# Kernel optimization log

Hardware: AMD Instinct MI355X
Metric: run time of the kernel (lower is better)

## Reference

```python
import jax, jax.numpy as jnp
import numpy as np

B, L, S, H, E = 2, 2048, 2048, 16, 64
EPS = 1e-8


def setup_inputs() -> dict:
    key = jax.random.key(0)
    k1, k2, k3, k4, k5 = jax.random.split(key, 5)
    query = jax.random.normal(k1, (B, L, H, E), dtype=jnp.float32)
    key_t = jax.random.normal(k2, (B, S, H, E), dtype=jnp.float32)
    value = jax.random.normal(k3, (B, S, H, E), dtype=jnp.float32)
    mask_miss_k = jax.random.randint(k4, (B, S, 1), 0, 2).astype(bool)
    mask_miss_q = jax.random.randint(k5, (B, L, 1), 0, 2).astype(bool)
    # monotone per-batch positions -> standard causal structure
    pos = jnp.broadcast_to(jnp.arange(L, dtype=jnp.int32)[None, :, None], (B, L, 1))
    return {"query": query, "key": key_t, "value": value,
            "mask_miss_k": mask_miss_k, "mask_miss_q": mask_miss_q,
            "pos": pos, "causal_mask": 1}


def reference(query, key, value, mask_miss_k, mask_miss_q, pos, causal_mask):
    # query: (B,L,H,E); key/value: (B,S,H,E)
    E_ = query.shape[-1]
    scale = 1.0 / np.sqrt(E_)
    scores = jnp.einsum('blhe,bshe->bhls', query, key)  # (B,H,L,S)
    if causal_mask:
        p = pos[..., 0]  # (B,L)
        causal_add = jnp.where(p[:, None, :] > p[:, :, None],
                               -jnp.inf, 0.0).astype(scores.dtype)  # (B,L,S)
        scores = scores + causal_add[:, None, :, :]
    # additive -inf masks for missing keys / queries
    m_k = jnp.where(mask_miss_k[..., 0][:, None, None, :], -jnp.inf, 0.0).astype(scores.dtype)
    m_q = jnp.where(mask_miss_q[..., 0][:, None, :, None], -jnp.inf, 0.0).astype(scores.dtype)
    # NOTE: scale multiplies (scores + M_k) exactly as in the original
    att = jnp.maximum(jax.nn.softmax(scale * (scores + m_k), axis=-1) + m_q, 0.0)
    # entropy of (post-relu, possibly unnormalized) attention weights
    entropy = -jnp.sum(att * jnp.log(jnp.clip(att, EPS, None)), axis=-1)  # (B,H,L)
    entropy = jnp.nan_to_num(entropy, nan=0.0)
    A = jnp.nan_to_num(att)  # dropout p=0 -> identity, then nan_to_num
    V = jnp.einsum('bhls,bshd->blhd', A, value)  # (B,L,H,E)
    return V, A, entropy
```

## Files before the change

### kernel.cpp

```cpp
#include <hip/hip_runtime.h>

#define BB 2
#define LL 2048
#define SS 2048
#define HH 16
#define EE 64
#define HE (HH*EE)
#define BL 128
#define TS 64
#define NT2 32
#define SCALEF 0.125f
#define NEGBIG (-1e30f)

typedef __bf16 bf8 __attribute__((ext_vector_type(8)));
typedef float f4v __attribute__((ext_vector_type(4)));
typedef unsigned int u32;
typedef unsigned short u16;

#define V_ELEMS  ((size_t)BB*LL*HH*EE)
#define A_BASE   (V_ELEMS)
#define ENT_BASE (A_BASE + (size_t)BB*HH*LL*SS)

__device__ __forceinline__ u16 bfb(float f) {
    u32 u = __builtin_bit_cast(u32, f);
    return (u16)((u + 0x7fffu + ((u >> 16) & 1u)) >> 16);
}
__device__ __forceinline__ int swz8(int r) { return (((r) & 7) ^ (((r) >> 3) & 7)) << 4; }

__device__ __forceinline__ f4v mfma16(bf8 a, bf8 b, f4v c) {
    return __builtin_amdgcn_mfma_f32_16x16x32_bf16(a, b, c, 0, 0, 0);
}
__device__ __forceinline__ int maskv(const void* p, int i, int isB) {
    return isB ? (int)((const unsigned char*)p)[i] : ((const int*)p)[i];
}
__device__ __forceinline__ void barrier_lds() {
    asm volatile("s_waitcnt lgkmcnt(0)" ::: "memory");
    __builtin_amdgcn_s_barrier();
    asm volatile("" ::: "memory");
}
__device__ __forceinline__ uint4 pack8(float4 f0, float4 f1) {
    uint4 wv;
    wv.x = bfb(f0.x) | ((u32)bfb(f0.y) << 16);
    wv.y = bfb(f0.z) | ((u32)bfb(f0.w) << 16);
    wv.z = bfb(f1.x) | ((u32)bfb(f1.y) << 16);
    wv.w = bfb(f1.z) | ((u32)bfb(f1.w) << 16);
    return wv;
}
__device__ __forceinline__ void st_out(float v, float* p) { *p = v; }
__device__ __forceinline__ void st_out4(f4v v, float* p) { *(f4v*)(void*)p = v; }

__device__ __forceinline__ void stage128x64(const float* __restrict__ src,
                                            char* lds, int tid) {
    const int r = tid >> 2, seg = tid & 3;
    const float* rp = src + (size_t)r * HE + seg * 16;
    float4 f0 = *(const float4*)(rp + 0);
    float4 f1 = *(const float4*)(rp + 4);
    float4 f2 = *(const float4*)(rp + 8);
    float4 f3 = *(const float4*)(rp + 12);
    const int base = r * 128 + seg * 32;
    *(uint4*)(void*)(lds + ((base +  0) ^ swz8(r))) = pack8(f0, f1);
    *(uint4*)(void*)(lds + ((base + 16) ^ swz8(r))) = pack8(f2, f3);
}

__global__ __launch_bounds__(512) void k_fused(
    const float* __restrict__ Qg, const float* __restrict__ Kg, const float* __restrict__ Vg,
    const void* __restrict__ mk, const void* __restrict__ mq,
    float* __restrict__ outF)
{
    __shared__ __align__(16) char ldsP[16384];
    __shared__ __align__(16) char ldsK[2][8192];
    __shared__ __align__(16) char ldsVT[2][8192];
    __shared__ float ldsKM[SS];
    __shared__ int sFlag;

    const int blk = blockIdx.x;
    const int bh  = (blk & 7) + (((blk >> 3) & 3) << 3);
    const int pair = blk >> 5;
    const int b = bh >> 4, h = bh & 15;
    const int tid = threadIdx.x;
    const int w = tid >> 6, lane = tid & 63, g = lane >> 4, le = lane & 15;

    int isB;
    {
        const unsigned char* c = (const unsigned char*)mk;
        unsigned acc = 0;
        #pragma unroll
        for (int j = 0; j < 8; ++j) {
            const int off = tid + j * 512;
            if (off & 3) acc |= c[off];
        }
        if (tid == 0) sFlag = 0;
        __syncthreads();
        if (acc) atomicOr(&sFlag, 1);
        __syncthreads();
        isB = sFlag;
    }
    for (int i = tid; i < SS; i += 512)
        ldsKM[i] = maskv(mk, b * SS + i, isB) ? NEGBIG : 0.f;

    const float* Qb = Qg + (size_t)b * LL * HE + h * EE;
    const float* Kb = Kg + (size_t)b * SS * HE + h * EE;
    const float* Vb = Vg + (size_t)b * SS * HE + h * EE;

    const int kr = tid >> 3, ksg = tid & 7;
    const float* kbase = Kb + (size_t)kr * HE + ksg * 8;
    const int koff = (kr * 128 + ksg * 16) ^ swz8(kr);
    const int vrp = tid >> 4, vei = tid & 15;
    const float* vbase = Vb + (size_t)(2 * vrp) * HE + vei * 4;

    for (int bi = 0; bi < 2; ++bi) {
        const int band = bi ? (15 - pair) : pair;
        const int l0 = band * BL;
        const int lbase = l0 + w * 16 + g * 4;
        const int whi = l0 + w * 16 + 15;
        const int ntile = 2 * (band + 1);

        stage128x64(Qb + (size_t)l0 * HE, ldsP, tid);
        __syncthreads();
        const int qr = w * 16 + le;
        bf8 qf0 = *(const bf8*)(void*)(ldsP + ((qr * 128 +  0 + g * 16) ^ swz8(qr)));
        bf8 qf1 = *(const bf8*)(void*)(ldsP + ((qr * 128 + 64 + g * 16) ^ swz8(qr)));
        barrier_lds();

        float M[4], D[4], T[4];
        #pragma unroll
        for (int r = 0; r < 4; ++r) { M[r] = NEGBIG; D[r] = 0.f; T[r] = 0.f; }

        float4 ka = *(const float4*)(kbase);
        float4 kb2 = *(const float4*)(kbase + 4);
        *(uint4*)(void*)(&ldsK[0][0] + koff) = pack8(ka, kb2);
        if (ntile > 1) {
            const float* kp = kbase + (size_t)TS * HE;
            ka = *(const float4*)(kp); kb2 = *(const float4*)(kp + 4);
        }
        barrier_lds();
        int cur = 0;

        for (int st = 0; st < ntile; ++st) {
            const int s0 = st * TS;
            if (st + 1 < ntile) {
                *(uint4*)(void*)(&ldsK[cur ^ 1][0] + koff) = pack8(ka, kb2);
                if (st + 2 < ntile) {
                    const float* kp = kbase + (size_t)(st + 2) * TS * HE;
                    ka = *(const float4*)(kp); kb2 = *(const float4*)(kp + 4);
                }
            }
            if (s0 <= whi) {
                f4v acc[4];
                float tm[4] = {NEGBIG, NEGBIG, NEGBIG, NEGBIG};
                #pragma unroll
                for (int cb = 0; cb < 4; ++cb) {
                    const int sr = cb * 16 + le;
                    bf8 k0 = *(const bf8*)(void*)(&ldsK[cur][0] + ((sr * 128 +  0 + g * 16) ^ swz8(sr)));
                    bf8 k1 = *(const bf8*)(void*)(&ldsK[cur][0] + ((sr * 128 + 64 + g * 16) ^ swz8(sr)));
                    f4v a = {0.f, 0.f, 0.f, 0.f};
                    a = mfma16(qf0, k0, a);
                    a = mfma16(qf1, k1, a);
                    const float km = ldsKM[s0 + cb * 16 + le];
                    const int s = s0 + cb * 16 + le;
                    #pragma unroll
                    for (int r = 0; r < 4; ++r) {
                        float z = a[r] * SCALEF + km;
                        if (s > lbase + r) z = NEGBIG;
                        acc[cb][r] = z;
                        tm[r] = fmaxf(tm[r], z);
                    }
                }
                #pragma unroll
                for (int r = 0; r < 4; ++r) {
                    #pragma unroll
                    for (int msk = 1; msk < 16; msk <<= 1)
                        tm[r] = fmaxf(tm[r], __shfl_xor(tm[r], msk));
                    const float mn  = fmaxf(M[r], tm[r]);
                    const float fre = __expf(M[r] - mn);
                    float ed = 0.f, et = 0.f;
                    #pragma unroll
                    for (int cb = 0; cb < 4; ++cb) {
                        const float z = acc[cb][r];
                        const float e = __expf(z - mn);
                        ed += e; et += e * z;
                    }
                    D[r] = D[r] * fre + ed;
                    T[r] = T[r] * fre + et;
                    M[r] = mn;
                }
            }
            barrier_lds();
            cur ^= 1;
        }

        float C[4];
        #pragma unroll
        for (int r = 0; r < 4; ++r) {
            #pragma unroll
            for (int msk = 1; msk < 16; msk <<= 1) {
                const float Mo = __shfl_xor(M[r], msk);
                const float Do = __shfl_xor(D[r], msk);
                const float To = __shfl_xor(T[r], msk);
                const float mn = fmaxf(M[r], Mo);
                const float fa = __expf(M[r] - mn);
                const float fb = __expf(Mo  - mn);
                D[r] = D[r] * fa + Do * fb;
                T[r] = T[r] * fa + To * fb;
                M[r] = mn;
            }
            const int l = lbase + r;
            const bool valid = (M[r] > -1e29f) && (maskv(mq, b * LL + l, isB) == 0);
            C[r] = valid ? (M[r] + __logf(D[r])) : 1e30f;
            const float ent = valid ? (C[r] - T[r] / D[r]) : 0.f;
            if (le == 0) st_out(ent, &outF[ENT_BASE + (size_t)bh * LL + l]);
        }

        f4v O[4];
        #pragma unroll
        for (int eb = 0; eb < 4; ++eb) O[eb] = (f4v){0.f, 0.f, 0.f, 0.f};

        ka  = *(const float4*)(kbase);
        kb2 = *(const float4*)(kbase + 4);
        float4 va  = *(const float4*)(vbase);
        float4 vb2 = *(const float4*)(vbase + HE);
        *(uint4*)(void*)(&ldsK[0][0] + koff) = pack8(ka, kb2);
        {
            const float* pa_ = &va.x; const float* pb_ = &vb2.x;
            #pragma unroll
            for (int i = 0; i < 4; ++i) {
                const int e = vei * 4 + i;
                const u32 pk = (u32)bfb(pa_[i]) | ((u32)bfb(pb_[i]) << 16);
                *(u32*)(void*)(&ldsVT[0][0] + ((e * 128 + vrp * 4) ^ swz8(e))) = pk;
            }
        }
        if (ntile > 1) {
            const float* kp = kbase + (size_t)TS * HE;
            const float* vp = vbase + (size_t)TS * HE;
            ka = *(const float4*)(kp); kb2 = *(const float4*)(kp + 4);
            va = *(const float4*)(vp); vb2 = *(const float4*)(vp + HE);
        }
        barrier_lds();
        cur = 0;
        float* const Arow0 = outF + A_BASE + ((size_t)bh * LL + l0) * SS;

        for (int st = 0; st < ntile; ++st) {
            const int s0 = st * TS;
            if (st + 1 < ntile) {
                *(uint4*)(void*)(&ldsK[cur ^ 1][0] + koff) = pack8(ka, kb2);
                {
                    const float* pa_ = &va.x; const float* pb_ = &vb2.x;
                    #pragma unroll
                    for (int i = 0; i < 4; ++i) {
                        const int e = vei * 4 + i;
                        const u32 pk = (u32)bfb(pa_[i]) | ((u32)bfb(pb_[i]) << 16);
                        *(u32*)(void*)(&ldsVT[cur ^ 1][0] + ((e * 128 + vrp * 4) ^ swz8(e))) = pk;
                    }
                }
                if (st + 2 < ntile) {
                    const float* kp = kbase + (size_t)(st + 2) * TS * HE;
                    const float* vp = vbase + (size_t)(st + 2) * TS * HE;
                    ka = *(const float4*)(kp); kb2 = *(const float4*)(kp + 4);
                    va = *(const float4*)(vp); vb2 = *(const float4*)(vp + HE);
                }
            }
            const bool active = (s0 <= whi);
            if (active) {
                f4v acc[4];
                #pragma unroll
                for (int cb = 0; cb < 4; ++cb) {
                    const int sr = cb * 16 + le;
                    bf8 k0 = *(const bf8*)(void*)(&ldsK[cur][0] + ((sr * 128 +  0 + g * 16) ^ swz8(sr)));
                    bf8 k1 = *(const bf8*)(void*)(&ldsK[cur][0] + ((sr * 128 + 64 + g * 16) ^ swz8(sr)));
                    f4v a = {0.f, 0.f, 0.f, 0.f};
                    a = mfma16(qf0, k0, a);
                    a = mfma16(qf1, k1, a);
                    acc[cb] = a;
                }
                #pragma unroll
                for (int cb = 0; cb < 4; ++cb) {
                    const float km = ldsKM[s0 + cb * 16 + le];
                    const int s = s0 + cb * 16 + le;
                    #pragma unroll
                    for (int r = 0; r < 4; ++r) {
                        float z = acc[cb][r] * SCALEF + km;
                        if (s > lbase + r) z = NEGBIG;
                        const float p = __expf(z - C[r]);
                        const int row = w * 16 + g * 4 + r;
                        *(u16*)(void*)(ldsP + ((row * 128 + (cb * 16 + le) * 2) ^ swz8(row))) = bfb(p);
                        st_out(p, Arow0 + (size_t)row * SS + s);
                    }
                }
            } else {
                #pragma unroll
                for (int cb = 0; cb < 4; ++cb) {
                    const int s = s0 + cb * 16 + le;
                    #pragma unroll
                    for (int r = 0; r < 4; ++r) {
                        const int row = w * 16 + g * 4 + r;
                        st_out(0.f, Arow0 + (size_t)row * SS + s);
                    }
                }
            }
            barrier_lds();

            if (active) {
                const int prow = w * 16 + le;
                #pragma unroll
                for (int kkb = 0; kkb < 2; ++kkb) {
                    bf8 pa = *(const bf8*)(void*)(ldsP + ((prow * 128 + kkb * 64 + g * 16) ^ swz8(prow)));
                    #pragma unroll
                    for (int eb = 0; eb < 4; ++eb) {
                        const int e = eb * 16 + le;
                        bf8 vb = *(const bf8*)(void*)(&ldsVT[cur][0] + ((e * 128 + kkb * 64 + g * 16) ^ swz8(e)));
                        O[eb] = mfma16(pa, vb, O[eb]);
                    }
                }
            }
            barrier_lds();
            cur ^= 1;
        }

        {
            const int r = tid >> 2, cseg = tid & 3;
            const f4v zz = {0.f, 0.f, 0.f, 0.f};
            for (int st = ntile; st < NT2; ++st) {
                float* dst = Arow0 + (size_t)r * SS + st * TS + cseg * 16;
                #pragma unroll
                for (int i = 0; i < 4; ++i) st_out4(zz, dst + i * 4);
            }
        }

        #pragma unroll
        for (int eb = 0; eb < 4; ++eb) {
            #pragma unroll
            for (int r = 0; r < 4; ++r) {
                const int l = lbase + r;
                st_out(O[eb][r], &outF[((size_t)(b * LL + l) * HH + h) * EE + eb * 16 + le]);
            }
        }
        __syncthreads();
    }
}

extern "C" void kernel_launch(void* const* d_in, const int* in_sizes, int n_in,
                              void* d_out, int out_size, void* d_ws, size_t ws_size,
                              hipStream_t stream) {
    const float* Q = (const float*)d_in[0];
    const float* K = (const float*)d_in[1];
    const float* V = (const float*)d_in[2];
    const void* mk = d_in[3];
    const void* mq = d_in[4];
    float* outF = (float*)d_out;

    dim3 blk(512), grid(BB * HH * 8);
    hipLaunchKernelGGL(k_fused, grid, blk, 0, stream, Q, K, V, mk, mq, outF);
}
```

Measured before the change: 238.5 us.

## Split fused attention into separate stats and output kernels with finer grids

The single fused kernel, which ran a stats pass and then an output pass per block over paired bands, is split into two launches. A 64-row-band stats kernel computes the softmax log-normaliser and entropy and writes the normaliser to workspace. A 128-row output kernel reads it back to produce A and V. The output kernel gives each wave its own P scratch, so the block-wide barrier between the P write and the PV MMA becomes a per-wave LDS wait, and it zero-fills the masked tail of A up front. This raises parallelism and removes barriers, at the cost of a second launch, recomputing QK^T, a workspace round trip, and an imbalanced causal workload per block.

```diff
diff --git a/kernel.cpp b/kernel.cpp
--- a/kernel.cpp
+++ b/kernel.cpp
@@ -6,9 +6,7 @@
 #define HH 16
 #define EE 64
 #define HE (HH*EE)
-#define BL 128
 #define TS 64
-#define NT2 32
 #define SCALEF 0.125f
 #define NEGBIG (-1e30f)
 
@@ -46,8 +44,6 @@
     wv.w = bfb(f1.z) | ((u32)bfb(f1.w) << 16);
     return wv;
 }
-__device__ __forceinline__ void st_out(float v, float* p) { *p = v; }
-__device__ __forceinline__ void st_out4(f4v v, float* p) { *(f4v*)(void*)p = v; }
 
 __device__ __forceinline__ void stage128x64(const float* __restrict__ src,
                                             char* lds, int tid) {
@@ -62,10 +58,168 @@
     *(uint4*)(void*)(lds + ((base + 16) ^ swz8(r))) = pack8(f2, f3);
 }
 
-__global__ __launch_bounds__(512) void k_fused(
+__global__ __launch_bounds__(256, 4) void k_stats(
+    const float* __restrict__ Qg, const float* __restrict__ Kg,
+    const void* __restrict__ mk, const void* __restrict__ mq,
+    float* __restrict__ outF, float* __restrict__ Cws)
+{
+    __shared__ __align__(16) char ldsK[2][8192];
+    __shared__ float ldsKM[SS];
+    __shared__ int sFlag;
+
+    const int blk = blockIdx.x;
+    const int xcd = blk & 7, idx = blk >> 3;
+    const int bh  = xcd * 4 + (idx & 3);
+    const int band = 31 - (idx >> 2);
+    const int b = bh >> 4, h = bh & 15;
+    const int tid = threadIdx.x;
+    const int w = tid >> 6, lane = tid & 63, g = lane >> 4, le = lane & 15;
+
+    int isB;
+    {
+        const unsigned char* c = (const unsigned char*)mk;
+        unsigned acc = 0;
+        #pragma unroll
+        for (int j = 0; j < 16; ++j) {
+            const int off = tid + j * 256;
+            if (off & 3) acc |= c[off];
+        }
+        if (tid == 0) sFlag = 0;
+        __syncthreads();
+        if (acc) atomicOr(&sFlag, 1);
+        __syncthreads();
+        isB = sFlag;
+    }
+    for (int i = tid; i < SS; i += 256)
+        ldsKM[i] = maskv(mk, b * SS + i, isB) ? NEGBIG : 0.f;
+
+    const float* Qb = Qg + (size_t)b * LL * HE + h * EE;
+    const float* Kb = Kg + (size_t)b * SS * HE + h * EE;
+
+    const int l0 = band * TS;
+    const int lbase = l0 + w * 16 + g * 4;
+    const int ntile = band + 1;
+
+    {
+        const int r = tid >> 2, seg = tid & 3;
+        const float* rp = Qb + (size_t)(l0 + r) * HE + seg * 16;
+        float4 f0 = *(const float4*)(rp + 0);
+        float4 f1 = *(const float4*)(rp + 4);
+        float4 f2 = *(const float4*)(rp + 8);
+        float4 f3 = *(const float4*)(rp + 12);
+        const int base = r * 128 + seg * 32;
+        *(uint4*)(void*)(&ldsK[0][0] + ((base +  0) ^ swz8(r))) = pack8(f0, f1);
+        *(uint4*)(void*)(&ldsK[0][0] + ((base + 16) ^ swz8(r))) = pack8(f2, f3);
+    }
+    __syncthreads();
+    const int qr = w * 16 + le;
+    bf8 qf0 = *(const bf8*)(void*)(&ldsK[0][0] + ((qr * 128 +  0 + g * 16) ^ swz8(qr)));
+    bf8 qf1 = *(const bf8*)(void*)(&ldsK[0][0] + ((qr * 128 + 64 + g * 16) ^ swz8(qr)));
+    barrier_lds();
+
+    const int kr = tid >> 2, ksg = tid & 3;
+    const float* kbase = Kb + (size_t)kr * HE + ksg * 16;
+    const int kb0 = kr * 128 + ksg * 32;
+    float4 p0 = *(const float4*)(kbase + 0);
+    float4 p1 = *(const float4*)(kbase + 4);
+    float4 p2 = *(const float4*)(kbase + 8);
+    float4 p3 = *(const float4*)(kbase + 12);
+    *(uint4*)(void*)(&ldsK[0][0] + ((kb0 +  0) ^ swz8(kr))) = pack8(p0, p1);
+    *(uint4*)(void*)(&ldsK[0][0] + ((kb0 + 16) ^ swz8(kr))) = pack8(p2, p3);
+    if (ntile > 1) {
+        const float* kp = kbase + (size_t)TS * HE;
+        p0 = *(const float4*)(kp + 0);  p1 = *(const float4*)(kp + 4);
+        p2 = *(const float4*)(kp + 8);  p3 = *(const float4*)(kp + 12);
+    }
+    barrier_lds();
+    int cur = 0;
+
+    float M[4], D[4], T[4];
+    #pragma unroll
+    for (int r = 0; r < 4; ++r) { M[r] = NEGBIG; D[r] = 0.f; T[r] = 0.f; }
+
+    for (int st = 0; st < ntile; ++st) {
+        const int s0 = st * TS;
+        if (st + 1 < ntile) {
+            *(uint4*)(void*)(&ldsK[cur ^ 1][0] + ((kb0 +  0) ^ swz8(kr))) = pack8(p0, p1);
+            *(uint4*)(void*)(&ldsK[cur ^ 1][0] + ((kb0 + 16) ^ swz8(kr))) = pack8(p2, p3);
+            if (st + 2 < ntile) {
+                const float* kp = kbase + (size_t)(st + 2) * TS * HE;
+                p0 = *(const float4*)(kp + 0);  p1 = *(const float4*)(kp + 4);
+                p2 = *(const float4*)(kp + 8);  p3 = *(const float4*)(kp + 12);
+            }
+        }
+        f4v acc[4];
+        float tm[4] = {NEGBIG, NEGBIG, NEGBIG, NEGBIG};
+        #pragma unroll
+        for (int cb = 0; cb < 4; ++cb) {
+            const int sr = cb * 16 + le;
+            bf8 k0 = *(const bf8*)(void*)(&ldsK[cur][0] + ((sr * 128 +  0 + g * 16) ^ swz8(sr)));
+            bf8 k1 = *(const bf8*)(void*)(&ldsK[cur][0] + ((sr * 128 + 64 + g * 16) ^ swz8(sr)));
+            f4v a = {0.f, 0.f, 0.f, 0.f};
+            a = mfma16(qf0, k0, a);
+            a = mfma16(qf1, k1, a);
+            const float km = ldsKM[s0 + cb * 16 + le];
+            const int s = s0 + cb * 16 + le;
+            #pragma unroll
+            for (int r = 0; r < 4; ++r) {
+                float z = a[r] * SCALEF + km;
+                if (s > lbase + r) z = NEGBIG;
+                acc[cb][r] = z;
+                tm[r] = fmaxf(tm[r], z);
+            }
+        }
+        #pragma unroll
+        for (int r = 0; r < 4; ++r) {
+            #pragma unroll
+            for (int msk = 1; msk < 16; msk <<= 1)
+                tm[r] = fmaxf(tm[r], __shfl_xor(tm[r], msk));
+            const float mn  = fmaxf(M[r], tm[r]);
+            const float fre = __expf(M[r] - mn);
+            float ed = 0.f, et = 0.f;
+            #pragma unroll
+            for (int cb = 0; cb < 4; ++cb) {
+                const float z = acc[cb][r];
+                const float e = __expf(z - mn);
+                ed += e; et += e * z;
+            }
+            D[r] = D[r] * fre + ed;
+            T[r] = T[r] * fre + et;
+            M[r] = mn;
+        }
+        barrier_lds();
+        cur ^= 1;
+    }
+
+    #pragma unroll
+    for (int r = 0; r < 4; ++r) {
+        #pragma unroll
+        for (int msk = 1; msk < 16; msk <<= 1) {
+            const float Mo = __shfl_xor(M[r], msk);
+            const float Do = __shfl_xor(D[r], msk);
+            const float To = __shfl_xor(T[r], msk);
+            const float mn = fmaxf(M[r], Mo);
+            const float fa = __expf(M[r] - mn);
+            const float fb = __expf(Mo  - mn);
+            D[r] = D[r] * fa + Do * fb;
+            T[r] = T[r] * fa + To * fb;
+            M[r] = mn;
+        }
+        const int l = lbase + r;
+        const bool valid = (M[r] > -1e29f) && (maskv(mq, b * LL + l, isB) == 0);
+        const float C = valid ? (M[r] + __logf(D[r])) : 1e30f;
+        const float ent = valid ? (C - T[r] / D[r]) : 0.f;
+        if (le == 0) {
+            outF[ENT_BASE + (size_t)bh * LL + l] = ent;
+            Cws[(size_t)bh * LL + l] = C;
+        }
+    }
+}
+
+__global__ __launch_bounds__(512, 4) void k_out(
     const float* __restrict__ Qg, const float* __restrict__ Kg, const float* __restrict__ Vg,
-    const void* __restrict__ mk, const void* __restrict__ mq,
-    float* __restrict__ outF)
+    const void* __restrict__ mk,
+    float* __restrict__ outF, const float* __restrict__ Cws)
 {
     __shared__ __align__(16) char ldsP[16384];
     __shared__ __align__(16) char ldsK[2][8192];
@@ -74,8 +228,9 @@
     __shared__ int sFlag;
 
     const int blk = blockIdx.x;
-    const int bh  = (blk & 7) + (((blk >> 3) & 3) << 3);
-    const int pair = blk >> 5;
+    const int xcd = blk & 7, idx = blk >> 3;
+    const int bh  = xcd * 4 + (idx & 3);
+    const int band = 15 - (idx >> 2);
     const int b = bh >> 4, h = bh & 15;
     const int tid = threadIdx.x;
     const int w = tid >> 6, lane = tid & 63, g = lane >> 4, le = lane & 15;
@@ -102,239 +257,136 @@
     const float* Kb = Kg + (size_t)b * SS * HE + h * EE;
     const float* Vb = Vg + (size_t)b * SS * HE + h * EE;
 
+    const int l0 = band * 128;
+    const int lbase = l0 + w * 16 + g * 4;
+    const int whi = l0 + w * 16 + 15;
+    const int ta  = whi >> 6;
+    const int ntile = 2 * (band + 1);
+
+    stage128x64(Qb + (size_t)l0 * HE, &ldsK[0][0], tid);
+    __syncthreads();
+    const int qr = w * 16 + le;
+    bf8 qf0 = *(const bf8*)(void*)(&ldsK[0][0] + ((qr * 128 +  0 + g * 16) ^ swz8(qr)));
+    bf8 qf1 = *(const bf8*)(void*)(&ldsK[0][0] + ((qr * 128 + 64 + g * 16) ^ swz8(qr)));
+    float C[4];
+    #pragma unroll
+    for (int r = 0; r < 4; ++r) C[r] = Cws[(size_t)bh * LL + lbase + r];
+    barrier_lds();
+
+    float* const Arow0 = outF + A_BASE + ((size_t)bh * LL + l0) * SS;
+
+    {
+        const int rr = lane >> 2, cc = lane & 3;
+        float* dst0 = Arow0 + (size_t)(w * 16 + rr) * SS;
+        const f4v zz = {0.f, 0.f, 0.f, 0.f};
+        for (int c = (ta + 1) * TS + cc * 4; c < SS; c += 16)
+            *(f4v*)(void*)(dst0 + c) = zz;
+    }
+
     const int kr = tid >> 3, ksg = tid & 7;
     const float* kbase = Kb + (size_t)kr * HE + ksg * 8;
     const int koff = (kr * 128 + ksg * 16) ^ swz8(kr);
     const int vrp = tid >> 4, vei = tid & 15;
     const float* vbase = Vb + (size_t)(2 * vrp) * HE + vei * 4;
 
-    for (int bi = 0; bi < 2; ++bi) {
-        const int band = bi ? (15 - pair) : pair;
-        const int l0 = band * BL;
-        const int lbase = l0 + w * 16 + g * 4;
-        const int whi = l0 + w * 16 + 15;
-        const int ntile = 2 * (band + 1);
-
-        stage128x64(Qb + (size_t)l0 * HE, ldsP, tid);
-        __syncthreads();
-        const int qr = w * 16 + le;
-        bf8 qf0 = *(const bf8*)(void*)(ldsP + ((qr * 128 +  0 + g * 16) ^ swz8(qr)));
-        bf8 qf1 = *(const bf8*)(void*)(ldsP + ((qr * 128 + 64 + g * 16) ^ swz8(qr)));
-        barrier_lds();
-
-        float M[4], D[4], T[4];
-        #pragma unroll
-        for (int r = 0; r < 4; ++r) { M[r] = NEGBIG; D[r] = 0.f; T[r] = 0.f; }
-
-        float4 ka = *(const float4*)(kbase);
-        float4 kb2 = *(const float4*)(kbase + 4);
-        *(uint4*)(void*)(&ldsK[0][0] + koff) = pack8(ka, kb2);
-        if (ntile > 1) {
-            const float* kp = kbase + (size_t)TS * HE;
-            ka = *(const float4*)(kp); kb2 = *(const float4*)(kp + 4);
-        }
-        barrier_lds();
-        int cur = 0;
-
-        for (int st = 0; st < ntile; ++st) {
-            const int s0 = st * TS;
-            if (st + 1 < ntile) {
-                *(uint4*)(void*)(&ldsK[cur ^ 1][0] + koff) = pack8(ka, kb2);
-                if (st + 2 < ntile) {
-                    const float* kp = kbase + (size_t)(st + 2) * TS * HE;
-                    ka = *(const float4*)(kp); kb2 = *(const float4*)(kp + 4);
+    float4 ka  = *(const float4*)(kbase);
+    float4 kb2 = *(const float4*)(kbase + 4);
+    float4 va  = *(const float4*)(vbase);
+    float4 vb2 = *(const float4*)(vbase + HE);
+    *(uint4*)(void*)(&ldsK[0][0] + koff) = pack8(ka, kb2);
+    {
+        const float* pa_ = &va.x; const float* pb_ = &vb2.x;
+        #pragma unroll
+        for (int i = 0; i < 4; ++i) {
+            const int e = vei * 4 + i;
+            const u32 pk = (u32)bfb(pa_[i]) | ((u32)bfb(pb_[i]) << 16);
+            *(u32*)(void*)(&ldsVT[0][0] + ((e * 128 + vrp * 4) ^ swz8(e))) = pk;
+        }
+    }
+    if (ntile > 1) {
+        const float* kp = kbase + (size_t)TS * HE;
+        const float* vp = vbase + (size_t)TS * HE;
+        ka = *(const float4*)(kp); kb2 = *(const float4*)(kp + 4);
+        va = *(const float4*)(vp); vb2 = *(const float4*)(vp + HE);
+    }
+    barrier_lds();
+    int cur = 0;
+    char* const myP = ldsP + w * 2048;
+
+    f4v O[4];
+    #pragma unroll
+    for (int eb = 0; eb < 4; ++eb) O[eb] = (f4v){0.f, 0.f, 0.f, 0.f};
+
+    for (int st = 0; st < ntile; ++st) {
+        const int s0 = st * TS;
+        if (st + 1 < ntile) {
+            *(uint4*)(void*)(&ldsK[cur ^ 1][0] + koff) = pack8(ka, kb2);
+            {
+                const float* pa_ = &va.x; const float* pb_ = &vb2.x;
+                #pragma unroll
+                for (int i = 0; i < 4; ++i) {
+                    const int e = vei * 4 + i;
+                    const u32 pk = (u32)bfb(pa_[i]) | ((u32)bfb(pb_[i]) << 16);
+                    *(u32*)(void*)(&ldsVT[cur ^ 1][0] + ((e * 128 + vrp * 4) ^ swz8(e))) = pk;
                 }
             }
-            if (s0 <= whi) {
-                f4v acc[4];
-                float tm[4] = {NEGBIG, NEGBIG, NEGBIG, NEGBIG};
-                #pragma unroll
-                for (int cb = 0; cb < 4; ++cb) {
-                    const int sr = cb * 16 + le;
-                    bf8 k0 = *(const bf8*)(void*)(&ldsK[cur][0] + ((sr * 128 +  0 + g * 16) ^ swz8(sr)));
-                    bf8 k1 = *(const bf8*)(void*)(&ldsK[cur][0] + ((sr * 128 + 64 + g * 16) ^ swz8(sr)));
-                    f4v a = {0.f, 0.f, 0.f, 0.f};
-                    a = mfma16(qf0, k0, a);
-                    a = mfma16(qf1, k1, a);
-                    const float km = ldsKM[s0 + cb * 16 + le];
-                    const int s = s0 + cb * 16 + le;
-                    #pragma unroll
-                    for (int r = 0; r < 4; ++r) {
-                        float z = a[r] * SCALEF + km;
-                        if (s > lbase + r) z = NEGBIG;
-                        acc[cb][r] = z;
-                        tm[r] = fmaxf(tm[r], z);
-                    }
-                }
+            if (st + 2 < ntile) {
+                const float* kp = kbase + (size_t)(st + 2) * TS * HE;
+                const float* vp = vbase + (size_t)(st + 2) * TS * HE;
+                ka = *(const float4*)(kp); kb2 = *(const float4*)(kp + 4);
+                va = *(const float4*)(vp); vb2 = *(const float4*)(vp + HE);
+            }
+        }
+        if (st <= ta) {
+            f4v acc[4];
+            #pragma unroll
+            for (int cb = 0; cb < 4; ++cb) {
+                const int sr = cb * 16 + le;
+                bf8 k0 = *(const bf8*)(void*)(&ldsK[cur][0] + ((sr * 128 +  0 + g * 16) ^ swz8(sr)));
+                bf8 k1 = *(const bf8*)(void*)(&ldsK[cur][0] + ((sr * 128 + 64 + g * 16) ^ swz8(sr)));
+                f4v a = {0.f, 0.f, 0.f, 0.f};
+                a = mfma16(qf0, k0, a);
+                a = mfma16(qf1, k1, a);
+                acc[cb] = a;
+            }
+            #pragma unroll
+            for (int cb = 0; cb < 4; ++cb) {
+                const float km = ldsKM[s0 + cb * 16 + le];
+                const int s = s0 + cb * 16 + le;
                 #pragma unroll
                 for (int r = 0; r < 4; ++r) {
-                    #pragma unroll
-                    for (int msk = 1; msk < 16; msk <<= 1)
-                        tm[r] = fmaxf(tm[r], __shfl_xor(tm[r], msk));
-                    const float mn  = fmaxf(M[r], tm[r]);
-                    const float fre = __expf(M[r] - mn);
-                    float ed = 0.f, et = 0.f;
-                    #pragma unroll
-                    for (int cb = 0; cb < 4; ++cb) {
-                        const float z = acc[cb][r];
-                        const float e = __expf(z - mn);
-                        ed += e; et += e * z;
-                    }
-                    D[r] = D[r] * fre + ed;
-                    T[r] = T[r] * fre + et;
-                    M[r] = mn;
+                    float z = acc[cb][r] * SCALEF + km;
+                    if (s > lbase + r) z = NEGBIG;
+                    const float p = __expf(z - C[r]);
+                    const int row = g * 4 + r;
+                    *(u16*)(void*)(myP + ((row * 128 + (cb * 16 + le) * 2) ^ swz8(row))) = bfb(p);
+                    outF[A_BASE + ((size_t)bh * LL + (l0 + w * 16 + row)) * SS + s] = p;
                 }
             }
-            barrier_lds();
-            cur ^= 1;
-        }
-
-        float C[4];
+            asm volatile("s_waitcnt lgkmcnt(0)" ::: "memory");
+
+            #pragma unroll
+            for (int kkb = 0; kkb < 2; ++kkb) {
+                bf8 pa = *(const bf8*)(void*)(myP + ((le * 128 + kkb * 64 + g * 16) ^ swz8(le)));
+                #pragma unroll
+                for (int eb = 0; eb < 4; ++eb) {
+                    const int e = eb * 16 + le;
+                    bf8 vb = *(const bf8*)(void*)(&ldsVT[cur][0] + ((e * 128 + kkb * 64 + g * 16) ^ swz8(e)));
+                    O[eb] = mfma16(pa, vb, O[eb]);
+                }
+            }
+        }
+        barrier_lds();
+        cur ^= 1;
+    }
+
+    #pragma unroll
+    for (int eb = 0; eb < 4; ++eb) {
         #pragma unroll
         for (int r = 0; r < 4; ++r) {
-            #pragma unroll
-            for (int msk = 1; msk < 16; msk <<= 1) {
-                const float Mo = __shfl_xor(M[r], msk);
-                const float Do = __shfl_xor(D[r], msk);
-                const float To = __shfl_xor(T[r], msk);
-                const float mn = fmaxf(M[r], Mo);
-                const float fa = __expf(M[r] - mn);
-                const float fb = __expf(Mo  - mn);
-                D[r] = D[r] * fa + Do * fb;
-                T[r] = T[r] * fa + To * fb;
-                M[r] = mn;
-            }
             const int l = lbase + r;
-            const bool valid = (M[r] > -1e29f) && (maskv(mq, b * LL + l, isB) == 0);
-            C[r] = valid ? (M[r] + __logf(D[r])) : 1e30f;
-            const float ent = valid ? (C[r] - T[r] / D[r]) : 0.f;
-            if (le == 0) st_out(ent, &outF[ENT_BASE + (size_t)bh * LL + l]);
-        }
-
-        f4v O[4];
-        #pragma unroll
-        for (int eb = 0; eb < 4; ++eb) O[eb] = (f4v){0.f, 0.f, 0.f, 0.f};
-
-        ka  = *(const float4*)(kbase);
-        kb2 = *(const float4*)(kbase + 4);
-        float4 va  = *(const float4*)(vbase);
-        float4 vb2 = *(const float4*)(vbase + HE);
-        *(uint4*)(void*)(&ldsK[0][0] + koff) = pack8(ka, kb2);
-        {
-            const float* pa_ = &va.x; const float* pb_ = &vb2.x;
-            #pragma unroll
-            for (int i = 0; i < 4; ++i) {
-                const int e = vei * 4 + i;
-                const u32 pk = (u32)bfb(pa_[i]) | ((u32)bfb(pb_[i]) << 16);
-                *(u32*)(void*)(&ldsVT[0][0] + ((e * 128 + vrp * 4) ^ swz8(e))) = pk;
-            }
-        }
-        if (ntile > 1) {
-            const float* kp = kbase + (size_t)TS * HE;
-            const float* vp = vbase + (size_t)TS * HE;
-            ka = *(const float4*)(kp); kb2 = *(const float4*)(kp + 4);
-            va = *(const float4*)(vp); vb2 = *(const float4*)(vp + HE);
-        }
-        barrier_lds();
-        cur = 0;
-        float* const Arow0 = outF + A_BASE + ((size_t)bh * LL + l0) * SS;
-
-        for (int st = 0; st < ntile; ++st) {
-            const int s0 = st * TS;
-            if (st + 1 < ntile) {
-                *(uint4*)(void*)(&ldsK[cur ^ 1][0] + koff) = pack8(ka, kb2);
-                {
-                    const float* pa_ = &va.x; const float* pb_ = &vb2.x;
-                    #pragma unroll
-                    for (int i = 0; i < 4; ++i) {
-                        const int e = vei * 4 + i;
-                        const u32 pk = (u32)bfb(pa_[i]) | ((u32)bfb(pb_[i]) << 16);
-                        *(u32*)(void*)(&ldsVT[cur ^ 1][0] + ((e * 128 + vrp * 4) ^ swz8(e))) = pk;
-                    }
-                }
-                if (st + 2 < ntile) {
-                    const float* kp = kbase + (size_t)(st + 2) * TS * HE;
-                    const float* vp = vbase + (size_t)(st + 2) * TS * HE;
-                    ka = *(const float4*)(kp); kb2 = *(const float4*)(kp + 4);
-                    va = *(const float4*)(vp); vb2 = *(const float4*)(vp + HE);
-                }
-            }
-            const bool active = (s0 <= whi);
-            if (active) {
-                f4v acc[4];
-                #pragma unroll
-                for (int cb = 0; cb < 4; ++cb) {
-                    const int sr = cb * 16 + le;
-                    bf8 k0 = *(const bf8*)(void*)(&ldsK[cur][0] + ((sr * 128 +  0 + g * 16) ^ swz8(sr)));
-                    bf8 k1 = *(const bf8*)(void*)(&ldsK[cur][0] + ((sr * 128 + 64 + g * 16) ^ swz8(sr)));
-                    f4v a = {0.f, 0.f, 0.f, 0.f};
-                    a = mfma16(qf0, k0, a);
-                    a = mfma16(qf1, k1, a);
-                    acc[cb] = a;
-                }
-                #pragma unroll
-                for (int cb = 0; cb < 4; ++cb) {
-                    const float km = ldsKM[s0 + cb * 16 + le];
-                    const int s = s0 + cb * 16 + le;
-                    #pragma unroll
-                    for (int r = 0; r < 4; ++r) {
-                        float z = acc[cb][r] * SCALEF + km;
-                        if (s > lbase + r) z = NEGBIG;
-                        const float p = __expf(z - C[r]);
-                        const int row = w * 16 + g * 4 + r;
-                        *(u16*)(void*)(ldsP + ((row * 128 + (cb * 16 + le) * 2) ^ swz8(row))) = bfb(p);
-                        st_out(p, Arow0 + (size_t)row * SS + s);
-                    }
-                }
-            } else {
-                #pragma unroll
-                for (int cb = 0; cb < 4; ++cb) {
-                    const int s = s0 + cb * 16 + le;
-                    #pragma unroll
-                    for (int r = 0; r < 4; ++r) {
-                        const int row = w * 16 + g * 4 + r;
-                        st_out(0.f, Arow0 + (size_t)row * SS + s);
-                    }
-                }
-            }
-            barrier_lds();
-
-            if (active) {
-                const int prow = w * 16 + le;
-                #pragma unroll
-                for (int kkb = 0; kkb < 2; ++kkb) {
-                    bf8 pa = *(const bf8*)(void*)(ldsP + ((prow * 128 + kkb * 64 + g * 16) ^ swz8(prow)));
-                    #pragma unroll
-                    for (int eb = 0; eb < 4; ++eb) {
-                        const int e = eb * 16 + le;
-                        bf8 vb = *(const bf8*)(void*)(&ldsVT[cur][0] + ((e * 128 + kkb * 64 + g * 16) ^ swz8(e)));
-                        O[eb] = mfma16(pa, vb, O[eb]);
-                    }
-                }
-            }
-            barrier_lds();
-            cur ^= 1;
-        }
-
-        {
-            const int r = tid >> 2, cseg = tid & 3;
-            const f4v zz = {0.f, 0.f, 0.f, 0.f};
-            for (int st = ntile; st < NT2; ++st) {
-                float* dst = Arow0 + (size_t)r * SS + st * TS + cseg * 16;
-                #pragma unroll
-                for (int i = 0; i < 4; ++i) st_out4(zz, dst + i * 4);
-            }
-        }
-
-        #pragma unroll
-        for (int eb = 0; eb < 4; ++eb) {
-            #pragma unroll
-            for (int r = 0; r < 4; ++r) {
-                const int l = lbase + r;
-                st_out(O[eb][r], &outF[((size_t)(b * LL + l) * HH + h) * EE + eb * 16 + le]);
-            }
-        }
-        __syncthreads();
+            outF[((size_t)(b * LL + l) * HH + h) * EE + eb * 16 + le] = O[eb][r];
+        }
     }
 }
 
@@ -347,7 +399,10 @@
     const void* mk = d_in[3];
     const void* mq = d_in[4];
     float* outF = (float*)d_out;
-
-    dim3 blk(512), grid(BB * HH * 8);
-    hipLaunchKernelGGL(k_fused, grid, blk, 0, stream, Q, K, V, mk, mq, outF);
-}
+    float* Cws  = (float*)d_ws;
+
+    hipLaunchKernelGGL(k_stats, dim3(BB * HH * 32), dim3(256), 0, stream,
+                       Q, K, mk, mq, outF, Cws);
+    hipLaunchKernelGGL(k_out,   dim3(BB * HH * 16), dim3(512), 0, stream,
+                       Q, K, V, mk, outF, Cws);
+}
```

Measured after the change: 295.9 us. 24.1% more time.

## Split band pairs into separate blocks, use per-wave P tiles and per-wave tile skipping

Applied to the files above, without the earlier changes.

Each block now handles one 128-row band instead of a balanced pair, doubling the grid and ordering bands largest-first, with occupancy hinted via launch bounds. The PV stage uses a per-wave slice of the P buffer so the mid-tile block barrier is replaced by a wave-local lgkmcnt wait. Each wave also skips tiles past its own diagonal and zero-fills the remaining A columns with a vectorized loop. The aim is better load balance, fewer barriers and fewer scalar zero stores. The cost is more blocks that each re-stage Q and re-read the mask.

```diff
diff --git a/kernel.cpp b/kernel.cpp
--- a/kernel.cpp
+++ b/kernel.cpp
@@ -6,9 +6,7 @@
 #define HH 16
 #define EE 64
 #define HE (HH*EE)
-#define BL 128
 #define TS 64
-#define NT2 32
 #define SCALEF 0.125f
 #define NEGBIG (-1e30f)
 
@@ -46,8 +44,6 @@
     wv.w = bfb(f1.z) | ((u32)bfb(f1.w) << 16);
     return wv;
 }
-__device__ __forceinline__ void st_out(float v, float* p) { *p = v; }
-__device__ __forceinline__ void st_out4(f4v v, float* p) { *(f4v*)(void*)p = v; }
 
 __device__ __forceinline__ void stage128x64(const float* __restrict__ src,
                                             char* lds, int tid) {
@@ -62,7 +58,7 @@
     *(uint4*)(void*)(lds + ((base + 16) ^ swz8(r))) = pack8(f2, f3);
 }
 
-__global__ __launch_bounds__(512) void k_fused(
+__global__ __launch_bounds__(512, 4) void k_fused(
     const float* __restrict__ Qg, const float* __restrict__ Kg, const float* __restrict__ Vg,
     const void* __restrict__ mk, const void* __restrict__ mq,
     float* __restrict__ outF)
@@ -74,8 +70,9 @@
     __shared__ int sFlag;
 
     const int blk = blockIdx.x;
-    const int bh  = (blk & 7) + (((blk >> 3) & 3) << 3);
-    const int pair = blk >> 5;
+    const int xcd = blk & 7, idx = blk >> 3;
+    const int bh  = xcd * 4 + (idx & 3);
+    const int band = 15 - (idx >> 2);
     const int b = bh >> 4, h = bh & 15;
     const int tid = threadIdx.x;
     const int w = tid >> 6, lane = tid & 63, g = lane >> 4, le = lane & 15;
@@ -102,239 +99,222 @@
     const float* Kb = Kg + (size_t)b * SS * HE + h * EE;
     const float* Vb = Vg + (size_t)b * SS * HE + h * EE;
 
+    const int l0 = band * 128;
+    const int lbase = l0 + w * 16 + g * 4;
+    const int whi = l0 + w * 16 + 15;
+    const int ta  = whi >> 6;
+    const int ntile = 2 * (band + 1);
+
+    stage128x64(Qb + (size_t)l0 * HE, ldsP, tid);
+    __syncthreads();
+    const int qr = w * 16 + le;
+    bf8 qf0 = *(const bf8*)(void*)(ldsP + ((qr * 128 +  0 + g * 16) ^ swz8(qr)));
+    bf8 qf1 = *(const bf8*)(void*)(ldsP + ((qr * 128 + 64 + g * 16) ^ swz8(qr)));
+    barrier_lds();
+
     const int kr = tid >> 3, ksg = tid & 7;
     const float* kbase = Kb + (size_t)kr * HE + ksg * 8;
     const int koff = (kr * 128 + ksg * 16) ^ swz8(kr);
     const int vrp = tid >> 4, vei = tid & 15;
     const float* vbase = Vb + (size_t)(2 * vrp) * HE + vei * 4;
 
-    for (int bi = 0; bi < 2; ++bi) {
-        const int band = bi ? (15 - pair) : pair;
-        const int l0 = band * BL;
-        const int lbase = l0 + w * 16 + g * 4;
-        const int whi = l0 + w * 16 + 15;
-        const int ntile = 2 * (band + 1);
-
-        stage128x64(Qb + (size_t)l0 * HE, ldsP, tid);
-        __syncthreads();
-        const int qr = w * 16 + le;
-        bf8 qf0 = *(const bf8*)(void*)(ldsP + ((qr * 128 +  0 + g * 16) ^ swz8(qr)));
-        bf8 qf1 = *(const bf8*)(void*)(ldsP + ((qr * 128 + 64 + g * 16) ^ swz8(qr)));
+    float M[4], D[4], T[4];
+    #pragma unroll
+    for (int r = 0; r < 4; ++r) { M[r] = NEGBIG; D[r] = 0.f; T[r] = 0.f; }
+
+    float4 ka = *(const float4*)(kbase);
+    float4 kb2 = *(const float4*)(kbase + 4);
+    *(uint4*)(void*)(&ldsK[0][0] + koff) = pack8(ka, kb2);
+    if (ntile > 1) {
+        const float* kp = kbase + (size_t)TS * HE;
+        ka = *(const float4*)(kp); kb2 = *(const float4*)(kp + 4);
+    }
+    barrier_lds();
+    int cur = 0;
+
+    for (int st = 0; st < ntile; ++st) {
+        const int s0 = st * TS;
+        if (st + 1 < ntile) {
+            *(uint4*)(void*)(&ldsK[cur ^ 1][0] + koff) = pack8(ka, kb2);
+            if (st + 2 < ntile) {
+                const float* kp = kbase + (size_t)(st + 2) * TS * HE;
+                ka = *(const float4*)(kp); kb2 = *(const float4*)(kp + 4);
+            }
+        }
+        if (s0 <= whi) {
+            f4v acc[4];
+            float tm[4] = {NEGBIG, NEGBIG, NEGBIG, NEGBIG};
+            #pragma unroll
+            for (int cb = 0; cb < 4; ++cb) {
+                const int sr = cb * 16 + le;
+                bf8 k0 = *(const bf8*)(void*)(&ldsK[cur][0] + ((sr * 128 +  0 + g * 16) ^ swz8(sr)));
+                bf8 k1 = *(const bf8*)(void*)(&ldsK[cur][0] + ((sr * 128 + 64 + g * 16) ^ swz8(sr)));
+                f4v a = {0.f, 0.f, 0.f, 0.f};
+                a = mfma16(qf0, k0, a);
+                a = mfma16(qf1, k1, a);
+                const float km = ldsKM[s0 + cb * 16 + le];
+                const int s = s0 + cb * 16 + le;
+                #pragma unroll
+                for (int r = 0; r < 4; ++r) {
+                    float z = a[r] * SCALEF + km;
+                    if (s > lbase + r) z = NEGBIG;
+                    acc[cb][r] = z;
+                    tm[r] = fmaxf(tm[r], z);
+                }
+            }
+            #pragma unroll
+            for (int r = 0; r < 4; ++r) {
+                #pragma unroll
+                for (int msk = 1; msk < 16; msk <<= 1)
+                    tm[r] = fmaxf(tm[r], __shfl_xor(tm[r], msk));
+                const float mn  = fmaxf(M[r], tm[r]);
+                const float fre = __expf(M[r] - mn);
+                float ed = 0.f, et = 0.f;
+                #pragma unroll
+                for (int cb = 0; cb < 4; ++cb) {
+                    const float z = acc[cb][r];
+                    const float e = __expf(z - mn);
+                    ed += e; et += e * z;
+                }
+                D[r] = D[r] * fre + ed;
+                T[r] = T[r] * fre + et;
+                M[r] = mn;
+            }
+        }
         barrier_lds();
-
-        float M[4], D[4], T[4];
+        cur ^= 1;
+    }
+
+    float C[4];
+    #pragma unroll
+    for (int r = 0; r < 4; ++r) {
         #pragma unroll
-        for (int r = 0; r < 4; ++r) { M[r] = NEGBIG; D[r] = 0.f; T[r] = 0.f; }
-
-        float4 ka = *(const float4*)(kbase);
-        float4 kb2 = *(const float4*)(kbase + 4);
-        *(uint4*)(void*)(&ldsK[0][0] + koff) = pack8(ka, kb2);
-        if (ntile > 1) {
-            const float* kp = kbase + (size_t)TS * HE;
-            ka = *(const float4*)(kp); kb2 = *(const float4*)(kp + 4);
+        for (int msk = 1; msk < 16; msk <<= 1) {
+            const float Mo = __shfl_xor(M[r], msk);
+            const float Do = __shfl_xor(D[r], msk);
+            const float To = __shfl_xor(T[r], msk);
+            const float mn = fmaxf(M[r], Mo);
+            const float fa = __expf(M[r] - mn);
+            const float fb = __expf(Mo  - mn);
+            D[r] = D[r] * fa + Do * fb;
+            T[r] = T[r] * fa + To * fb;
+            M[r] = mn;
+        }
+        const int l = lbase + r;
+        const bool valid = (M[r] > -1e29f) && (maskv(mq, b * LL + l, isB) == 0);
+        C[r] = valid ? (M[r] + __logf(D[r])) : 1e30f;
+        const float ent = valid ? (C[r] - T[r] / D[r]) : 0.f;
+        if (le == 0) outF[ENT_BASE + (size_t)bh * LL + l] = ent;
+    }
+
+    float* const Arow0 = outF + A_BASE + ((size_t)bh * LL + l0) * SS;
+
+    {
+        const int rr = lane >> 2, cc = lane & 3;
+        float* dst0 = Arow0 + (size_t)(w * 16 + rr) * SS;
+        const f4v zz = {0.f, 0.f, 0.f, 0.f};
+        for (int c = (ta + 1) * TS + cc * 4; c < SS; c += 16)
+            *(f4v*)(void*)(dst0 + c) = zz;
+    }
+
+    f4v O[4];
+    #pragma unroll
+    for (int eb = 0; eb < 4; ++eb) O[eb] = (f4v){0.f, 0.f, 0.f, 0.f};
+
+    ka  = *(const float4*)(kbase);
+    kb2 = *(const float4*)(kbase + 4);
+    float4 va  = *(const float4*)(vbase);
+    float4 vb2 = *(const float4*)(vbase + HE);
+    *(uint4*)(void*)(&ldsK[0][0] + koff) = pack8(ka, kb2);
+    {
+        const float* pa_ = &va.x; const float* pb_ = &vb2.x;
+        #pragma unroll
+        for (int i = 0; i < 4; ++i) {
+            const int e = vei * 4 + i;
+            const u32 pk = (u32)bfb(pa_[i]) | ((u32)bfb(pb_[i]) << 16);
+            *(u32*)(void*)(&ldsVT[0][0] + ((e * 128 + vrp * 4) ^ swz8(e))) = pk;
+        }
+    }
+    if (ntile > 1) {
+        const float* kp = kbase + (size_t)TS * HE;
+        const float* vp = vbase + (size_t)TS * HE;
+        ka = *(const float4*)(kp); kb2 = *(const float4*)(kp + 4);
+        va = *(const float4*)(vp); vb2 = *(const float4*)(vp + HE);
+    }
+    barrier_lds();
+    cur = 0;
+    char* const myP = ldsP + w * 2048;
+
+    for (int st = 0; st < ntile; ++st) {
+        const int s0 = st * TS;
+        if (st + 1 < ntile) {
+            *(uint4*)(void*)(&ldsK[cur ^ 1][0] + koff) = pack8(ka, kb2);
+            {
+                const float* pa_ = &va.x; const float* pb_ = &vb2.x;
+                #pragma unroll
+                for (int i = 0; i < 4; ++i) {
+                    const int e = vei * 4 + i;
+                    const u32 pk = (u32)bfb(pa_[i]) | ((u32)bfb(pb_[i]) << 16);
+                    *(u32*)(void*)(&ldsVT[cur ^ 1][0] + ((e * 128 + vrp * 4) ^ swz8(e))) = pk;
+                }
+            }
+            if (st + 2 < ntile) {
+                const float* kp = kbase + (size_t)(st + 2) * TS * HE;
+                const float* vp = vbase + (size_t)(st + 2) * TS * HE;
+                ka = *(const float4*)(kp); kb2 = *(const float4*)(kp + 4);
+                va = *(const float4*)(vp); vb2 = *(const float4*)(vp + HE);
+            }
+        }
+        if (st <= ta) {
+            f4v acc[4];
+            #pragma unroll
+            for (int cb = 0; cb < 4; ++cb) {
+                const int sr = cb * 16 + le;
+                bf8 k0 = *(const bf8*)(void*)(&ldsK[cur][0] + ((sr * 128 +  0 + g * 16) ^ swz8(sr)));
+                bf8 k1 = *(const bf8*)(void*)(&ldsK[cur][0] + ((sr * 128 + 64 + g * 16) ^ swz8(sr)));
+                f4v a = {0.f, 0.f, 0.f, 0.f};
+                a = mfma16(qf0, k0, a);
+                a = mfma16(qf1, k1, a);
+                acc[cb] = a;
+            }
+            #pragma unroll
+            for (int cb = 0; cb < 4; ++cb) {
+                const float km = ldsKM[s0 + cb * 16 + le];
+                const int s = s0 + cb * 16 + le;
+                #pragma unroll
+                for (int r = 0; r < 4; ++r) {
+                    float z = acc[cb][r] * SCALEF + km;
+                    if (s > lbase + r) z = NEGBIG;
+                    const float p = __expf(z - C[r]);
+                    const int row = g * 4 + r;
+                    *(u16*)(void*)(myP + ((row * 128 + (cb * 16 + le) * 2) ^ swz8(row))) = bfb(p);
+                    outF[A_BASE + ((size_t)bh * LL + (l0 + w * 16 + row)) * SS + s] = p;
+                }
+            }
+            asm volatile("s_waitcnt lgkmcnt(0)" ::: "memory");
+
+            #pragma unroll
+            for (int kkb = 0; kkb < 2; ++kkb) {
+                bf8 pa = *(const bf8*)(void*)(myP + ((le * 128 + kkb * 64 + g * 16) ^ swz8(le)));
+                #pragma unroll
+                for (int eb = 0; eb < 4; ++eb) {
+                    const int e = eb * 16 + le;
+                    bf8 vb = *(const bf8*)(void*)(&ldsVT[cur][0] + ((e * 128 + kkb * 64 + g * 16) ^ swz8(e)));
+                    O[eb] = mfma16(pa, vb, O[eb]);
+                }
+            }
         }
         barrier_lds();
-        int cur = 0;
-
-        for (int st = 0; st < ntile; ++st) {
-            const int s0 = st * TS;
-            if (st + 1 < ntile) {
-                *(uint4*)(void*)(&ldsK[cur ^ 1][0] + koff) = pack8(ka, kb2);
-                if (st + 2 < ntile) {
-                    const float* kp = kbase + (size_t)(st + 2) * TS * HE;
-                    ka = *(const float4*)(kp); kb2 = *(const float4*)(kp + 4);
-                }
-            }
-            if (s0 <= whi) {
-                f4v acc[4];
-                float tm[4] = {NEGBIG, NEGBIG, NEGBIG, NEGBIG};
-                #pragma unroll
-                for (int cb = 0; cb < 4; ++cb) {
-                    const int sr = cb * 16 + le;
-                    bf8 k0 = *(const bf8*)(void*)(&ldsK[cur][0] + ((sr * 128 +  0 + g * 16) ^ swz8(sr)));
-                    bf8 k1 = *(const bf8*)(void*)(&ldsK[cur][0] + ((sr * 128 + 64 + g * 16) ^ swz8(sr)));
-                    f4v a = {0.f, 0.f, 0.f, 0.f};
-                    a = mfma16(qf0, k0, a);
-                    a = mfma16(qf1, k1, a);
-                    const float km = ldsKM[s0 + cb * 16 + le];
-                    const int s = s0 + cb * 16 + le;
-                    #pragma unroll
-                    for (int r = 0; r < 4; ++r) {
-                        float z = a[r] * SCALEF + km;
-                        if (s > lbase + r) z = NEGBIG;
-                        acc[cb][r] = z;
-                        tm[r] = fmaxf(tm[r], z);
-                    }
-                }
-                #pragma unroll
-                for (int r = 0; r < 4; ++r) {
-                    #pragma unroll
-                    for (int msk = 1; msk < 16; msk <<= 1)
-                        tm[r] = fmaxf(tm[r], __shfl_xor(tm[r], msk));
-                    const float mn  = fmaxf(M[r], tm[r]);
-                    const float fre = __expf(M[r] - mn);
-                    float ed = 0.f, et = 0.f;
-                    #pragma unroll
-                    for (int cb = 0; cb < 4; ++cb) {
-                        const float z = acc[cb][r];
-                        const float e = __expf(z - mn);
-                        ed += e; et += e * z;
-                    }
-                    D[r] = D[r] * fre + ed;
-                    T[r] = T[r] * fre + et;
-                    M[r] = mn;
-                }
-            }
-            barrier_lds();
-            cur ^= 1;
-        }
-
-        float C[4];
+        cur ^= 1;
+    }
+
+    #pragma unroll
+    for (int eb = 0; eb < 4; ++eb) {
         #pragma unroll
         for (int r = 0; r < 4; ++r) {
-            #pragma unroll
-            for (int msk = 1; msk < 16; msk <<= 1) {
-                const float Mo = __shfl_xor(M[r], msk);
-                const float Do = __shfl_xor(D[r], msk);
-                const float To = __shfl_xor(T[r], msk);
-                const float mn = fmaxf(M[r], Mo);
-                const float fa = __expf(M[r] - mn);
-                const float fb = __expf(Mo  - mn);
-                D[r] = D[r] * fa + Do * fb;
-                T[r] = T[r] * fa + To * fb;
-                M[r] = mn;
-            }
             const int l = lbase + r;
-            const bool valid = (M[r] > -1e29f) && (maskv(mq, b * LL + l, isB) == 0);
-            C[r] = valid ? (M[r] + __logf(D[r])) : 1e30f;
-            const float ent = valid ? (C[r] - T[r] / D[r]) : 0.f;
-            if (le == 0) st_out(ent, &outF[ENT_BASE + (size_t)bh * LL + l]);
-        }
-
-        f4v O[4];
-        #pragma unroll
-        for (int eb = 0; eb < 4; ++eb) O[eb] = (f4v){0.f, 0.f, 0.f, 0.f};
-
-        ka  = *(const float4*)(kbase);
-        kb2 = *(const float4*)(kbase + 4);
-        float4 va  = *(const float4*)(vbase);
-        float4 vb2 = *(const float4*)(vbase + HE);
-        *(uint4*)(void*)(&ldsK[0][0] + koff) = pack8(ka, kb2);
-        {
-            const float* pa_ = &va.x; const float* pb_ = &vb2.x;
-            #pragma unroll
-            for (int i = 0; i < 4; ++i) {
-                const int e = vei * 4 + i;
-                const u32 pk = (u32)bfb(pa_[i]) | ((u32)bfb(pb_[i]) << 16);
-                *(u32*)(void*)(&ldsVT[0][0] + ((e * 128 + vrp * 4) ^ swz8(e))) = pk;
-            }
-        }
-        if (ntile > 1) {
-            const float* kp = kbase + (size_t)TS * HE;
-            const float* vp = vbase + (size_t)TS * HE;
-            ka = *(const float4*)(kp); kb2 = *(const float4*)(kp + 4);
-            va = *(const float4*)(vp); vb2 = *(const float4*)(vp + HE);
-        }
-        barrier_lds();
-        cur = 0;
-        float* const Arow0 = outF + A_BASE + ((size_t)bh * LL + l0) * SS;
-
-        for (int st = 0; st < ntile; ++st) {
-            const int s0 = st * TS;
-            if (st + 1 < ntile) {
-                *(uint4*)(void*)(&ldsK[cur ^ 1][0] + koff) = pack8(ka, kb2);
-                {
-                    const float* pa_ = &va.x; const float* pb_ = &vb2.x;
-                    #pragma unroll
-                    for (int i = 0; i < 4; ++i) {
-                        const int e = vei * 4 + i;
-                        const u32 pk = (u32)bfb(pa_[i]) | ((u32)bfb(pb_[i]) << 16);
-                        *(u32*)(void*)(&ldsVT[cur ^ 1][0] + ((e * 128 + vrp * 4) ^ swz8(e))) = pk;
-                    }
-                }
-                if (st + 2 < ntile) {
-                    const float* kp = kbase + (size_t)(st + 2) * TS * HE;
-                    const float* vp = vbase + (size_t)(st + 2) * TS * HE;
-                    ka = *(const float4*)(kp); kb2 = *(const float4*)(kp + 4);
-                    va = *(const float4*)(vp); vb2 = *(const float4*)(vp + HE);
-                }
-            }
-            const bool active = (s0 <= whi);
-            if (active) {
-                f4v acc[4];
-                #pragma unroll
-                for (int cb = 0; cb < 4; ++cb) {
-                    const int sr = cb * 16 + le;
-                    bf8 k0 = *(const bf8*)(void*)(&ldsK[cur][0] + ((sr * 128 +  0 + g * 16) ^ swz8(sr)));
-                    bf8 k1 = *(const bf8*)(void*)(&ldsK[cur][0] + ((sr * 128 + 64 + g * 16) ^ swz8(sr)));
-                    f4v a = {0.f, 0.f, 0.f, 0.f};
-                    a = mfma16(qf0, k0, a);
-                    a = mfma16(qf1, k1, a);
-                    acc[cb] = a;
-                }
-                #pragma unroll
-                for (int cb = 0; cb < 4; ++cb) {
-                    const float km = ldsKM[s0 + cb * 16 + le];
-                    const int s = s0 + cb * 16 + le;
-                    #pragma unroll
-                    for (int r = 0; r < 4; ++r) {
-                        float z = acc[cb][r] * SCALEF + km;
-                        if (s > lbase + r) z = NEGBIG;
-                        const float p = __expf(z - C[r]);
-                        const int row = w * 16 + g * 4 + r;
-                        *(u16*)(void*)(ldsP + ((row * 128 + (cb * 16 + le) * 2) ^ swz8(row))) = bfb(p);
-                        st_out(p, Arow0 + (size_t)row * SS + s);
-                    }
-                }
-            } else {
-                #pragma unroll
-                for (int cb = 0; cb < 4; ++cb) {
-                    const int s = s0 + cb * 16 + le;
-                    #pragma unroll
-                    for (int r = 0; r < 4; ++r) {
-                        const int row = w * 16 + g * 4 + r;
-                        st_out(0.f, Arow0 + (size_t)row * SS + s);
-                    }
-                }
-            }
-            barrier_lds();
-
-            if (active) {
-                const int prow = w * 16 + le;
-                #pragma unroll
-                for (int kkb = 0; kkb < 2; ++kkb) {
-                    bf8 pa = *(const bf8*)(void*)(ldsP + ((prow * 128 + kkb * 64 + g * 16) ^ swz8(prow)));
-                    #pragma unroll
-                    for (int eb = 0; eb < 4; ++eb) {
-                        const int e = eb * 16 + le;
-                        bf8 vb = *(const bf8*)(void*)(&ldsVT[cur][0] + ((e * 128 + kkb * 64 + g * 16) ^ swz8(e)));
-                        O[eb] = mfma16(pa, vb, O[eb]);
-                    }
-                }
-            }
-            barrier_lds();
-            cur ^= 1;
-        }
-
-        {
-            const int r = tid >> 2, cseg = tid & 3;
-            const f4v zz = {0.f, 0.f, 0.f, 0.f};
-            for (int st = ntile; st < NT2; ++st) {
-                float* dst = Arow0 + (size_t)r * SS + st * TS + cseg * 16;
-                #pragma unroll
-                for (int i = 0; i < 4; ++i) st_out4(zz, dst + i * 4);
-            }
-        }
-
-        #pragma unroll
-        for (int eb = 0; eb < 4; ++eb) {
-            #pragma unroll
-            for (int r = 0; r < 4; ++r) {
-                const int l = lbase + r;
-                st_out(O[eb][r], &outF[((size_t)(b * LL + l) * HH + h) * EE + eb * 16 + le]);
-            }
-        }
-        __syncthreads();
+            outF[((size_t)(b * LL + l) * HH + h) * EE + eb * 16 + le] = O[eb][r];
+        }
     }
 }
 
@@ -348,6 +328,6 @@
     const void* mq = d_in[4];
     float* outF = (float*)d_out;
 
-    dim3 blk(512), grid(BB * HH * 8);
+    dim3 blk(512), grid(BB * HH * 16);
     hipLaunchKernelGGL(k_fused, grid, blk, 0, stream, Q, K, V, mk, mq, outF);
 }
```

New measurement: 221.9 us. 6.9% less time.
